# Kernel optimization log

Hardware: AMD Instinct MI355X
Metric: run time of the kernel (lower is better)

The kernel has to match this reference:

```python
import jax, jax.numpy as jnp
import numpy as np

D_MODEL = 512
N_HEADS = 8
D_HEAD = D_MODEL // N_HEADS
EPS = 1e-6


def setup_inputs() -> dict:
    key = jax.random.key(0)
    ks = jax.random.split(key, 9)
    B, S = 2, 2048
    scale = 0.02
    x = jax.random.normal(ks[0], (B, S, D_MODEL), dtype=jnp.float32)
    Wq = jax.random.normal(ks[1], (D_MODEL, D_MODEL), dtype=jnp.float32) * scale
    Wk = jax.random.normal(ks[2], (D_MODEL, D_MODEL), dtype=jnp.float32) * scale
    Wv = jax.random.normal(ks[3], (D_MODEL, D_MODEL), dtype=jnp.float32) * scale
    Wo = jax.random.normal(ks[4], (D_MODEL, D_MODEL), dtype=jnp.float32) * scale
    bq = jax.random.normal(ks[5], (D_MODEL,), dtype=jnp.float32) * scale
    bk = jax.random.normal(ks[6], (D_MODEL,), dtype=jnp.float32) * scale
    bv = jax.random.normal(ks[7], (D_MODEL,), dtype=jnp.float32) * scale
    bo = jax.random.normal(ks[8], (D_MODEL,), dtype=jnp.float32) * scale
    return {"x": x, "Wq": Wq, "bq": bq, "Wk": Wk, "bk": bk,
            "Wv": Wv, "bv": bv, "Wo": Wo, "bo": bo}


def _split_heads(t, B, S):
    # [B,S,D] -> [B,H,S,dh]
    return t.reshape(B, S, N_HEADS, D_HEAD).transpose(0, 2, 1, 3)


def reference(x, Wq, bq, Wk, bk, Wv, bv, Wo, bo):
    B, S, _ = x.shape
    q = _split_heads(x @ Wq.T + bq, B, S)
    k = _split_heads(x @ Wk.T + bk, B, S)
    v = _split_heads(x @ Wv.T + bv, B, S)
    # 'relu' kernel applied to Q and K
    q = jax.nn.relu(q)
    k = jax.nn.relu(k)
    # K_sum: [B,H,S,1] -- per-position sum over head dim; note it broadcasts
    # over the KEY axis of attn, i.e. each QUERY row n is divided by K_sum[n]
    k_sum = k.sum(axis=-1, keepdims=True)
    attn = jnp.einsum('bhnd,bhmd->bhnm', q, k) / (k_sum + EPS)
    attn = jax.nn.softmax(attn, axis=-1)
    out = jnp.einsum('bhnm,bhmd->bhnd', attn, v)
    out = out.transpose(0, 2, 1, 3).reshape(B, S, D_MODEL)
    return (out @ Wo.T + bo, attn)
```

## Files before the change

kernel.cpp:

```cpp
#include <hip/hip_runtime.h>
#include <stdint.h>


typedef __attribute__((ext_vector_type(8))) short short8;
typedef __attribute__((ext_vector_type(4))) float f4;

#define MFMA(a, b, c) __builtin_amdgcn_mfma_f32_16x16x32_bf16(a, b, c, 0, 0, 0)

struct __align__(8) us4 { uint16_t a, b, c, d; };

__device__ __forceinline__ uint16_t f2bf(float f) {
  union { float f; uint32_t u; } v; v.f = f;
  uint32_t u = v.u;
  return (uint16_t)((u + 0x7fffu + ((u >> 16) & 1u)) >> 16);
}
__device__ __forceinline__ float bf2f(uint16_t u) {
  union { uint32_t u; float f; } v; v.u = ((uint32_t)u) << 16; return v.f;
}
__device__ __forceinline__ us4 pack4(float4 v) {
  us4 r; r.a = f2bf(v.x); r.b = f2bf(v.y); r.c = f2bf(v.z); r.d = f2bf(v.w); return r;
}

__device__ __forceinline__ void async16(const uint16_t* g, uint16_t* l) {
  __builtin_amdgcn_global_load_lds(
      (const __attribute__((address_space(1))) void*)g,
      (__attribute__((address_space(3))) void*)l, 16, 0, 0);
}

__global__ __launch_bounds__(256) void convert_kernel(
    const float* __restrict__ x, const float* __restrict__ Wq,
    const float* __restrict__ Wk, const float* __restrict__ Wv,
    const float* __restrict__ Wo, uint16_t* __restrict__ xb,
    uint16_t* __restrict__ W3, uint16_t* __restrict__ Wob) {
  int i = blockIdx.x * 256 + threadIdx.x;
  ((us4*)xb)[i] = pack4(((const float4*)x)[i]);
  if (i < 65536) {
    ((us4*)W3)[i]          = pack4(((const float4*)Wq)[i]);
    ((us4*)W3)[65536 + i]  = pack4(((const float4*)Wk)[i]);
    ((us4*)W3)[131072 + i] = pack4(((const float4*)Wv)[i]);
    ((us4*)Wob)[i]         = pack4(((const float4*)Wo)[i]);
  }
}

__device__ __forceinline__ void gemm_loop(
    const uint16_t* __restrict__ A, const uint16_t* __restrict__ Bt,
    int row0, int col0, uint16_t* A0, uint16_t* B0,
    uint16_t* A1, uint16_t* B1, f4 (&acc)[4][4]) {
  const int tid = threadIdx.x;
  const int w = tid >> 6, lane = tid & 63;
  const int c = lane & 15, quad = lane >> 4;
  const int wm = w >> 1, wn = w & 1;
  const int srow = lane >> 2;
  const int sslot = ((lane & 3) ^ ((lane >> 2) & 3) ^ ((lane >> 4) & 3)) * 8;
  const uint16_t* Asrc = A + (size_t)(row0 + srow) * 512 + sslot;
  const uint16_t* Bsrc = Bt + (size_t)(col0 + srow) * 512 + sslot;
  const int posv = (quad ^ (c & 3) ^ (c >> 2)) * 8;
#pragma unroll
  for (int chh = 0; chh < 2; ++chh) {
    int ch = w * 2 + chh;
    async16(Asrc + (size_t)ch * 16 * 512, A0 + ch * 512);
    async16(Bsrc + (size_t)ch * 16 * 512, B0 + ch * 512);
  }
  __syncthreads();
  for (int k0 = 0; k0 < 512; k0 += 32) {
    const uint16_t* Ac = (k0 & 32) ? A1 : A0;
    const uint16_t* Bc = (k0 & 32) ? B1 : B0;
    if (k0 + 32 < 512) {
      uint16_t* An = (k0 & 32) ? A0 : A1;
      uint16_t* Bn = (k0 & 32) ? B0 : B1;
#pragma unroll
      for (int chh = 0; chh < 2; ++chh) {
        int ch = w * 2 + chh;
        async16(Asrc + (size_t)ch * 16 * 512 + (k0 + 32), An + ch * 512);
        async16(Bsrc + (size_t)ch * 16 * 512 + (k0 + 32), Bn + ch * 512);
      }
    }
    short8 af[4], bfr[4];
#pragma unroll
    for (int mi = 0; mi < 4; ++mi)
      af[mi] = *(const short8*)&Ac[(wm * 64 + mi * 16 + c) * 32 + posv];
#pragma unroll
    for (int ni = 0; ni < 4; ++ni)
      bfr[ni] = *(const short8*)&Bc[(wn * 64 + ni * 16 + c) * 32 + posv];
#pragma unroll
    for (int mi = 0; mi < 4; ++mi)
#pragma unroll
      for (int ni = 0; ni < 4; ++ni)
        acc[mi][ni] = MFMA(af[mi], bfr[ni], acc[mi][ni]);
    __syncthreads();
  }
}

__global__ __launch_bounds__(256) void qkv_gemm(
    const uint16_t* __restrict__ xb, const uint16_t* __restrict__ W3,
    const float* __restrict__ bq, const float* __restrict__ bk,
    const float* __restrict__ bv, uint16_t* __restrict__ Qb,
    uint16_t* __restrict__ Kb, uint16_t* __restrict__ Vt,
    float* __restrict__ rq) {
  __shared__ __align__(16) uint16_t smem[25600];
  uint16_t* A0 = smem;
  uint16_t* B0 = smem + 4096;
  uint16_t* A1 = smem + 8192;
  uint16_t* B1 = smem + 12288;
  uint16_t* Ct = smem + 8192;
  f4 acc[4][4] = {};
  const int row0 = blockIdx.y * 128, col0 = blockIdx.x * 128;
  gemm_loop(xb, W3, row0, col0, A0, B0, A1, B1, acc);
  const int tid = threadIdx.x, w = tid >> 6, lane = tid & 63;
  const int c = lane & 15, quad = lane >> 4;
  const int wm = w >> 1, wn = w & 1;
  const int r3 = col0 >> 9;
  if (r3 == 0) {
#pragma unroll
    for (int mi = 0; mi < 4; ++mi)
#pragma unroll
      for (int ni = 0; ni < 4; ++ni)
#pragma unroll
        for (int r = 0; r < 4; ++r) {
          int row = row0 + wm * 64 + mi * 16 + quad * 4 + r;
          int col = col0 + wn * 64 + ni * 16 + c;
          int o = col & 511;
          float v = acc[mi][ni][r] + bq[o];
          Qb[(size_t)row * 512 + o] = f2bf(fmaxf(v, 0.0f));
        }
  } else if (r3 == 1) {
    const int hh = ((col0 & 511) >> 6) + wn;
#pragma unroll
    for (int mi = 0; mi < 4; ++mi)
#pragma unroll
      for (int r = 0; r < 4; ++r) {
        int row = row0 + wm * 64 + mi * 16 + quad * 4 + r;
        float s = 0.f;
#pragma unroll
        for (int ni = 0; ni < 4; ++ni) {
          int col = col0 + wn * 64 + ni * 16 + c;
          int o = col & 511;
          float v = fmaxf(acc[mi][ni][r] + bk[o], 0.0f);
          Kb[(size_t)row * 512 + o] = f2bf(v);
          s += v;
        }
        s += __shfl_xor(s, 1, 16);
        s += __shfl_xor(s, 2, 16);
        s += __shfl_xor(s, 4, 16);
        s += __shfl_xor(s, 8, 16);
        if (c == 0) rq[(size_t)row * 8 + hh] = 1.0f / (s + 1e-6f);
      }
  } else {
#pragma unroll
    for (int mi = 0; mi < 4; ++mi)
#pragma unroll
      for (int ni = 0; ni < 4; ++ni)
#pragma unroll
        for (int r = 0; r < 4; ++r) {
          int sl = wm * 64 + mi * 16 + quad * 4 + r;
          int cl = wn * 64 + ni * 16 + c;
          int o = (col0 + cl) & 511;
          Ct[sl * 136 + cl] = f2bf(acc[mi][ni][r] + bv[o]);
        }
    __syncthreads();
    const int b = row0 >> 11, s0 = row0 & 2047;
    const int cl = tid >> 1, half = tid & 1;
    const int ocol = (col0 - 1024) + cl;
    uint16_t* vdst = Vt + (size_t)(b * 512 + ocol) * 2048 + s0 + half * 64;
#pragma unroll
    for (int g = 0; g < 8; ++g) {
      union { short8 v; uint16_t e[8]; } o8;
#pragma unroll
      for (int jj = 0; jj < 8; ++jj)
        o8.e[jj] = Ct[(half * 64 + g * 8 + jj) * 136 + cl];
      *(short8*)(vdst + g * 8) = o8.v;
    }
  }
}

__global__ __launch_bounds__(256) void proj_gemm(
    const uint16_t* __restrict__ Ob, const uint16_t* __restrict__ Wob,
    const float* __restrict__ bo, float* __restrict__ out) {
  __shared__ __align__(16) uint16_t smem[16384];
  uint16_t* A0 = smem;
  uint16_t* B0 = smem + 4096;
  uint16_t* A1 = smem + 8192;
  uint16_t* B1 = smem + 12288;
  f4 acc[4][4] = {};
  const int row0 = blockIdx.y * 128, col0 = blockIdx.x * 128;
  gemm_loop(Ob, Wob, row0, col0, A0, B0, A1, B1, acc);
  const int tid = threadIdx.x, w = tid >> 6, lane = tid & 63;
  const int c = lane & 15, quad = lane >> 4;
  const int wm = w >> 1, wn = w & 1;
#pragma unroll
  for (int mi = 0; mi < 4; ++mi)
#pragma unroll
    for (int ni = 0; ni < 4; ++ni)
#pragma unroll
      for (int r = 0; r < 4; ++r) {
        int row = row0 + wm * 64 + mi * 16 + quad * 4 + r;
        int col = col0 + wn * 64 + ni * 16 + c;
        out[(size_t)row * 512 + col] = acc[mi][ni][r] + bo[col];
      }
}

__global__ __launch_bounds__(256) void attn_kernel(
    const uint16_t* __restrict__ Qb, const uint16_t* __restrict__ Kb,
    const uint16_t* __restrict__ Vt, const float* __restrict__ rq,
    float* __restrict__ attn, uint16_t* __restrict__ Ob) {
  __shared__ __align__(16) uint16_t Klds[2][64 * 64];
  __shared__ __align__(16) uint16_t Vlds[2][64 * 64];
  __shared__ __align__(16) uint16_t Pw[4][16 * 64];
  const int tid = threadIdx.x, w = tid >> 6, lane = tid & 63;
  const int c = lane & 15, quad = lane >> 4, c7 = c & 7;
  const int bid = blockIdx.x;
  const int bh = (bid & 7) * 2 + ((bid >> 3) & 1);
  const int qt = bid >> 4;
  const int b = bh >> 3, h = bh & 7;
  const int n0 = qt * 64;
  const int rbase = b * 2048 + n0;
  const uint16_t* qptr = Qb + (size_t)(rbase + w * 16 + c) * 512 + h * 64 + quad * 8;
  short8 aq0 = *(const short8*)qptr;
  short8 aq1 = *(const short8*)(qptr + 32);
  const float rqv = rq[(size_t)(rbase + w * 16 + c) * 8 + h];
  const int vsrow = lane >> 3;
  const int vslot = ((lane & 7) ^ vsrow) * 8;
  const uint16_t* Ksrc = Kb + (size_t)(b * 2048) * 512 + h * 64 + vslot;
  const uint16_t* Vsrc = Vt + (size_t)(bh * 64) * 2048 + vslot;

  float lsum = 0.f;
#pragma unroll
  for (int chh = 0; chh < 2; ++chh) {
    int ch = w * 2 + chh;
    async16(Ksrc + (size_t)(ch * 8 + vsrow) * 512, Klds[0] + ch * 512);
  }
  __syncthreads();
  for (int kt = 0; kt < 32; ++kt) {
    const uint16_t* Kc = Klds[kt & 1];
    if (kt < 31) {
      uint16_t* Kn = Klds[(kt & 1) ^ 1];
#pragma unroll
      for (int chh = 0; chh < 2; ++chh) {
        int ch = w * 2 + chh;
        async16(Ksrc + (size_t)((kt + 1) * 64 + ch * 8 + vsrow) * 512,
                Kn + ch * 512);
      }
    }
#pragma unroll
    for (int ni = 0; ni < 4; ++ni) {
      const uint16_t* kp = &Kc[(ni * 16 + c) * 64];
      short8 bk0 = *(const short8*)(kp + ((quad ^ c7) * 8));
      short8 bk1 = *(const short8*)(kp + (((quad + 4) ^ c7) * 8));
      f4 s = {};
      s = MFMA(bk0, aq0, s);
      s = MFMA(bk1, aq1, s);
#pragma unroll
      for (int r = 0; r < 4; ++r) lsum += __expf(s[r] * rqv);
    }
    __syncthreads();
  }
  lsum += __shfl_xor(lsum, 16);
  lsum += __shfl_xor(lsum, 32);
  const float rli = 1.0f / lsum;

  f4 oacc[4] = {};
  float* arow = attn + ((size_t)bh * 2048 + n0 + w * 16 + c) * 2048;
  uint16_t* Pme = Pw[w];
#pragma unroll
  for (int chh = 0; chh < 2; ++chh) {
    int ch = w * 2 + chh;
    async16(Ksrc + (size_t)(ch * 8 + vsrow) * 512, Klds[0] + ch * 512);
    async16(Vsrc + (size_t)(ch * 8 + vsrow) * 2048, Vlds[0] + ch * 512);
  }
  __syncthreads();
  for (int kt = 0; kt < 32; ++kt) {
    const int cur = kt & 1;
    const uint16_t* Kc = Klds[cur];
    const uint16_t* Vc = Vlds[cur];
    if (kt < 31) {
      uint16_t* Kn = Klds[cur ^ 1];
      uint16_t* Vn = Vlds[cur ^ 1];
#pragma unroll
      for (int chh = 0; chh < 2; ++chh) {
        int ch = w * 2 + chh;
        async16(Ksrc + (size_t)((kt + 1) * 64 + ch * 8 + vsrow) * 512,
                Kn + ch * 512);
        async16(Vsrc + (size_t)(ch * 8 + vsrow) * 2048 + (kt + 1) * 64,
                Vn + ch * 512);
      }
    }
#pragma unroll
    for (int ni = 0; ni < 4; ++ni) {
      const uint16_t* kp = &Kc[(ni * 16 + c) * 64];
      short8 bk0 = *(const short8*)(kp + ((quad ^ c7) * 8));
      short8 bk1 = *(const short8*)(kp + (((quad + 4) ^ c7) * 8));
      f4 s = {};
      s = MFMA(bk0, aq0, s);
      s = MFMA(bk1, aq1, s);
      f4 p;
#pragma unroll
      for (int r = 0; r < 4; ++r) p[r] = __expf(s[r] * rqv) * rli;
      __builtin_nontemporal_store(p, (f4*)&arow[kt * 64 + ni * 16 + quad * 4]);
      uint32_t q01 = (uint32_t)f2bf(p[0]) | ((uint32_t)f2bf(p[1]) << 16);
      uint32_t q23 = (uint32_t)f2bf(p[2]) | ((uint32_t)f2bf(p[3]) << 16);
      int slot_w = (ni * 2 + (quad >> 1)) ^ c7;
      uint32_t* wp = (uint32_t*)&Pme[c * 64 + slot_w * 8 + (quad & 1) * 4];
      wp[0] = q01;
      wp[1] = q23;
    }
    asm volatile("s_waitcnt lgkmcnt(0)" ::: "memory");
#pragma unroll
    for (int m = 0; m < 2; ++m) {
      short8 pa = *(const short8*)&Pme[c * 64 + (((m * 4 + quad) ^ c7) * 8)];
#pragma unroll
      for (int nj = 0; nj < 4; ++nj) {
        short8 bvv = *(const short8*)&Vc[(nj * 16 + c) * 64 +
                                         (((m * 4 + quad) ^ c7) * 8)];
        oacc[nj] = MFMA(pa, bvv, oacc[nj]);
      }
    }
    __syncthreads();
  }
#pragma unroll
  for (int nj = 0; nj < 4; ++nj)
#pragma unroll
    for (int r = 0; r < 4; ++r)
      Ob[(size_t)(rbase + w * 16 + quad * 4 + r) * 512 + h * 64 + nj * 16 + c] =
          f2bf(oacc[nj][r]);
}

extern "C" void kernel_launch(void* const* d_in, const int* in_sizes, int n_in,
                              void* d_out, int out_size, void* d_ws, size_t ws_size,
                              hipStream_t stream) {
  const float* x  = (const float*)d_in[0];
  const float* Wq = (const float*)d_in[1];
  const float* bq = (const float*)d_in[2];
  const float* Wk = (const float*)d_in[3];
  const float* bk = (const float*)d_in[4];
  const float* Wv = (const float*)d_in[5];
  const float* bv = (const float*)d_in[6];
  const float* Wo = (const float*)d_in[7];
  const float* bo = (const float*)d_in[8];

  float* out0 = (float*)d_out;
  float* attn = out0 + (size_t)2 * 2048 * 512;

  uint8_t* ws = (uint8_t*)d_ws;
  uint16_t* xb  = (uint16_t*)(ws);
  uint16_t* W3  = (uint16_t*)(ws + 0x400000);
  uint16_t* Wob = (uint16_t*)(ws + 0x580000);
  uint16_t* Qb  = (uint16_t*)(ws + 0x600000);
  uint16_t* Kb  = (uint16_t*)(ws + 0xA00000);
  uint16_t* Vt  = (uint16_t*)(ws + 0xE00000);
  uint16_t* Ob  = (uint16_t*)(ws + 0x1200000);
  float*    rq  = (float*)  (ws + 0x1600000);

  convert_kernel<<<2048, 256, 0, stream>>>(x, Wq, Wk, Wv, Wo, xb, W3, Wob);
  qkv_gemm<<<dim3(12, 32), 256, 0, stream>>>(xb, W3, bq, bk, bv, Qb, Kb, Vt, rq);
  attn_kernel<<<512, 256, 0, stream>>>(Qb, Kb, Vt, rq, attn, Ob);
  proj_gemm<<<dim3(4, 32), 256, 0, stream>>>(Ob, Wob, bo, out0);
}
```

Measured before the change: 391.6 us.

## Split attention key range across two wave groups per block with LDS reduction

The attention block grows from 4 to 8 waves, and the two halves of the waves each process half of the key sequence (split-K) for the same 64 query rows. Row sums and output partials are combined through shared memory, and K/V tiles for both halves are loaded together into larger dynamic LDS buffers. This doubles the parallel waves per block to better hide exp and memory latency on the attention-matrix store path. The cost is more LDS (80KB, which may reduce blocks per CU), extra barriers and a final cross-wave reduction.

```diff
diff --git a/kernel.cpp b/kernel.cpp
--- a/kernel.cpp
+++ b/kernel.cpp
@@ -199,48 +199,49 @@
       }
 }
 
-__global__ __launch_bounds__(256) void attn_kernel(
+__global__ __launch_bounds__(512) void attn_kernel(
     const uint16_t* __restrict__ Qb, const uint16_t* __restrict__ Kb,
     const uint16_t* __restrict__ Vt, const float* __restrict__ rq,
     float* __restrict__ attn, uint16_t* __restrict__ Ob) {
-  __shared__ __align__(16) uint16_t Klds[2][64 * 64];
-  __shared__ __align__(16) uint16_t Vlds[2][64 * 64];
-  __shared__ __align__(16) uint16_t Pw[4][16 * 64];
+  extern __shared__ __align__(16) uint16_t smem[];
+  uint16_t* Klds = smem;
+  uint16_t* Vlds = smem + 16384;
+  uint16_t* Pw   = smem + 32768;
+  float* lsum_sh = (float*)(Vlds + 12288);
   const int tid = threadIdx.x, w = tid >> 6, lane = tid & 63;
   const int c = lane & 15, quad = lane >> 4, c7 = c & 7;
+  const int qsub = w & 3, kh = w >> 2;
   const int bid = blockIdx.x;
   const int bh = (bid & 7) * 2 + ((bid >> 3) & 1);
   const int qt = bid >> 4;
   const int b = bh >> 3, h = bh & 7;
   const int n0 = qt * 64;
   const int rbase = b * 2048 + n0;
-  const uint16_t* qptr = Qb + (size_t)(rbase + w * 16 + c) * 512 + h * 64 + quad * 8;
+  const int qrow = rbase + qsub * 16 + c;
+  const uint16_t* qptr = Qb + (size_t)qrow * 512 + h * 64 + quad * 8;
   short8 aq0 = *(const short8*)qptr;
   short8 aq1 = *(const short8*)(qptr + 32);
-  const float rqv = rq[(size_t)(rbase + w * 16 + c) * 8 + h];
+  const float rqv = rq[(size_t)qrow * 8 + h];
   const int vsrow = lane >> 3;
   const int vslot = ((lane & 7) ^ vsrow) * 8;
-  const uint16_t* Ksrc = Kb + (size_t)(b * 2048) * 512 + h * 64 + vslot;
-  const uint16_t* Vsrc = Vt + (size_t)(bh * 64) * 2048 + vslot;
-
+
+  const int t1 = w & 1, q8 = w >> 1;
+  const uint16_t* K1src =
+      Kb + (size_t)(b * 2048 + t1 * 1024 + q8 * 8 + vsrow) * 512 + h * 64 + vslot;
+  uint16_t* K1dst = Klds + t1 * 4096 + q8 * 512;
   float lsum = 0.f;
-#pragma unroll
-  for (int chh = 0; chh < 2; ++chh) {
-    int ch = w * 2 + chh;
-    async16(Ksrc + (size_t)(ch * 8 + vsrow) * 512, Klds[0] + ch * 512);
-  }
-  __syncthreads();
-  for (int kt = 0; kt < 32; ++kt) {
-    const uint16_t* Kc = Klds[kt & 1];
-    if (kt < 31) {
-      uint16_t* Kn = Klds[(kt & 1) ^ 1];
-#pragma unroll
-      for (int chh = 0; chh < 2; ++chh) {
-        int ch = w * 2 + chh;
-        async16(Ksrc + (size_t)((kt + 1) * 64 + ch * 8 + vsrow) * 512,
-                Kn + ch * 512);
-      }
-    }
+  async16(K1src, K1dst);
+  async16(K1src + (size_t)32 * 512, K1dst + 2048);
+  __syncthreads();
+  for (int it = 0; it < 16; ++it) {
+    const int cur = it & 1;
+    if (it < 15) {
+      const uint16_t* s = K1src + (size_t)(it + 1) * 64 * 512;
+      uint16_t* d = K1dst + (cur ^ 1) * 8192;
+      async16(s, d);
+      async16(s + (size_t)32 * 512, d + 2048);
+    }
+    const uint16_t* Kc = Klds + cur * 8192 + kh * 4096;
 #pragma unroll
     for (int ni = 0; ni < 4; ++ni) {
       const uint16_t* kp = &Kc[(ni * 16 + c) * 64];
@@ -256,34 +257,40 @@
   }
   lsum += __shfl_xor(lsum, 16);
   lsum += __shfl_xor(lsum, 32);
-  const float rli = 1.0f / lsum;
-
+  if (lane < 16) lsum_sh[w * 16 + c] = lsum;
+  __syncthreads();
+  const float rli =
+      1.0f / (lsum_sh[qsub * 16 + c] + lsum_sh[(qsub + 4) * 16 + c]);
+
+  const int t2 = w & 3, pair = w >> 2;
+  const bool isK = (t2 < 2);
+  const uint16_t* Gsrc = isK
+      ? Kb + (size_t)(b * 2048 + (t2 & 1) * 1024 + pair * 8 + vsrow) * 512 +
+            h * 64 + vslot
+      : Vt + (size_t)(bh * 64 + pair * 8 + vsrow) * 2048 + (t2 & 1) * 1024 +
+            vslot;
+  const size_t g_rr = isK ? (size_t)16 * 512 : (size_t)16 * 2048;
+  const size_t g_it = isK ? (size_t)64 * 512 : (size_t)64;
+  uint16_t* KV2dst = (isK ? Klds : Vlds) + (t2 & 1) * 4096 + pair * 512;
+#pragma unroll
+  for (int rr = 0; rr < 4; ++rr)
+    async16(Gsrc + rr * g_rr, KV2dst + rr * 1024);
+  __syncthreads();
   f4 oacc[4] = {};
-  float* arow = attn + ((size_t)bh * 2048 + n0 + w * 16 + c) * 2048;
-  uint16_t* Pme = Pw[w];
-#pragma unroll
-  for (int chh = 0; chh < 2; ++chh) {
-    int ch = w * 2 + chh;
-    async16(Ksrc + (size_t)(ch * 8 + vsrow) * 512, Klds[0] + ch * 512);
-    async16(Vsrc + (size_t)(ch * 8 + vsrow) * 2048, Vlds[0] + ch * 512);
-  }
-  __syncthreads();
-  for (int kt = 0; kt < 32; ++kt) {
-    const int cur = kt & 1;
-    const uint16_t* Kc = Klds[cur];
-    const uint16_t* Vc = Vlds[cur];
-    if (kt < 31) {
-      uint16_t* Kn = Klds[cur ^ 1];
-      uint16_t* Vn = Vlds[cur ^ 1];
-#pragma unroll
-      for (int chh = 0; chh < 2; ++chh) {
-        int ch = w * 2 + chh;
-        async16(Ksrc + (size_t)((kt + 1) * 64 + ch * 8 + vsrow) * 512,
-                Kn + ch * 512);
-        async16(Vsrc + (size_t)(ch * 8 + vsrow) * 2048 + (kt + 1) * 64,
-                Vn + ch * 512);
-      }
-    }
+  float* arow = attn + ((size_t)bh * 2048 + n0 + qsub * 16 + c) * 2048;
+  uint16_t* Pme = Pw + w * 1024;
+  const int colb = kh * 1024;
+  for (int it = 0; it < 16; ++it) {
+    const int cur = it & 1;
+    if (it < 15) {
+      const uint16_t* s = Gsrc + (size_t)(it + 1) * g_it;
+      uint16_t* d = KV2dst + (cur ^ 1) * 8192;
+#pragma unroll
+      for (int rr = 0; rr < 4; ++rr)
+        async16(s + rr * g_rr, d + rr * 1024);
+    }
+    const uint16_t* Kc = Klds + cur * 8192 + kh * 4096;
+    const uint16_t* Vc = Vlds + cur * 8192 + kh * 4096;
 #pragma unroll
     for (int ni = 0; ni < 4; ++ni) {
       const uint16_t* kp = &Kc[(ni * 16 + c) * 64];
@@ -295,7 +302,8 @@
       f4 p;
 #pragma unroll
       for (int r = 0; r < 4; ++r) p[r] = __expf(s[r] * rqv) * rli;
-      __builtin_nontemporal_store(p, (f4*)&arow[kt * 64 + ni * 16 + quad * 4]);
+      __builtin_nontemporal_store(
+          p, (f4*)&arow[colb + it * 64 + ni * 16 + quad * 4]);
       uint32_t q01 = (uint32_t)f2bf(p[0]) | ((uint32_t)f2bf(p[1]) << 16);
       uint32_t q23 = (uint32_t)f2bf(p[2]) | ((uint32_t)f2bf(p[3]) << 16);
       int slot_w = (ni * 2 + (quad >> 1)) ^ c7;
@@ -316,12 +324,26 @@
     }
     __syncthreads();
   }
-#pragma unroll
-  for (int nj = 0; nj < 4; ++nj)
-#pragma unroll
-    for (int r = 0; r < 4; ++r)
-      Ob[(size_t)(rbase + w * 16 + quad * 4 + r) * 512 + h * 64 + nj * 16 + c] =
-          f2bf(oacc[nj][r]);
+  float* Osh = (float*)Klds;
+  if (kh == 1) {
+#pragma unroll
+    for (int nj = 0; nj < 4; ++nj)
+#pragma unroll
+      for (int r = 0; r < 4; ++r)
+        Osh[(qsub * 16 + quad * 4 + r) * 64 + nj * 16 + c] = oacc[nj][r];
+  }
+  __syncthreads();
+  if (kh == 0) {
+#pragma unroll
+    for (int nj = 0; nj < 4; ++nj)
+#pragma unroll
+      for (int r = 0; r < 4; ++r) {
+        float v =
+            oacc[nj][r] + Osh[(qsub * 16 + quad * 4 + r) * 64 + nj * 16 + c];
+        Ob[(size_t)(rbase + qsub * 16 + quad * 4 + r) * 512 + h * 64 +
+           nj * 16 + c] = f2bf(v);
+      }
+  }
 }
 
 extern "C" void kernel_launch(void* const* d_in, const int* in_sizes, int n_in,
@@ -350,8 +372,15 @@
   uint16_t* Ob  = (uint16_t*)(ws + 0x1200000);
   float*    rq  = (float*)  (ws + 0x1600000);
 
+  static bool attr_set = false;
+  if (!attr_set) {
+    hipFuncSetAttribute((const void*)attn_kernel,
+                        hipFuncAttributeMaxDynamicSharedMemorySize, 81920);
+    attr_set = true;
+  }
+
   convert_kernel<<<2048, 256, 0, stream>>>(x, Wq, Wk, Wv, Wo, xb, W3, Wob);
   qkv_gemm<<<dim3(12, 32), 256, 0, stream>>>(xb, W3, bq, bk, bv, Qb, Kb, Vt, rq);
-  attn_kernel<<<512, 256, 0, stream>>>(Qb, Kb, Vt, rq, attn, Ob);
+  attn_kernel<<<512, 512, 81920, stream>>>(Qb, Kb, Vt, rq, attn, Ob);
   proj_gemm<<<dim3(4, 32), 256, 0, stream>>>(Ob, Wob, bo, out0);
 }
```

New measurement: 381.3 us. -2.6%, faster.
